# Performance work log

Measured on AMD Instinct MI355X. Metric: run time of the kernel, lower is better.

The kernel has to match this reference:

```python
import jax, jax.numpy as jnp
import numpy as np

VOCAB_SIZE = 32000
HIDDEN_DIM = 1024
NUM_BUF_ACTIONS = 128
BATCH = 64
SEQ_LEN = 512


def setup_inputs() -> dict:
    key = jax.random.key(0)
    ks = jax.random.split(key, 8)
    H = HIDDEN_DIM
    x = jax.random.randint(ks[0], (BATCH, SEQ_LEN), 0, VOCAB_SIZE, dtype=jnp.int32)
    true_actions = jax.random.randint(ks[1], (BATCH, SEQ_LEN), 0, NUM_BUF_ACTIONS, dtype=jnp.int32)
    true_states = jax.random.randint(ks[2], (BATCH, SEQ_LEN), 0, NUM_BUF_ACTIONS, dtype=jnp.int32)
    use_forcing = 0
    # Learned params: embedding table, LSTM input/recurrent kernels (gate order i,f,g,o), dense head
    embed = jax.random.normal(ks[3], (VOCAB_SIZE, H), dtype=jnp.float32) * 0.02
    Wi = jax.random.normal(ks[4], (H, 4 * H), dtype=jnp.float32) * (1.0 / np.sqrt(H))
    Wh = jax.random.normal(ks[5], (H, 4 * H), dtype=jnp.float32) * (1.0 / np.sqrt(H))
    bh = jnp.zeros((4 * H,), dtype=jnp.float32)
    Wo = jax.random.normal(ks[6], (H, NUM_BUF_ACTIONS), dtype=jnp.float32) * (1.0 / np.sqrt(H))
    bo = jnp.zeros((NUM_BUF_ACTIONS,), dtype=jnp.float32)
    return {"embed": embed, "Wi": Wi, "Wh": Wh, "bh": bh, "Wo": Wo, "bo": bo,
            "x": x, "true_actions": true_actions, "true_states": true_states,
            "use_forcing": use_forcing}


def _lstm_forward(embed, Wi, Wh, bh, Wo, bo, x):
    B, S = x.shape
    H = embed.shape[1]
    x_emb = embed[x]                                    # [B,S,H]
    # Precompute input-side gate projections for all timesteps (one big GEMM)
    gx = jnp.einsum('bsh,hg->sbg', x_emb, Wi)           # [S,B,4H]
    c0 = jnp.zeros((B, H), dtype=x_emb.dtype)
    h0 = jnp.zeros((B, H), dtype=x_emb.dtype)

    def step(carry, gx_t):
        c, h = carry
        gates = gx_t + h @ Wh + bh                      # [B,4H]
        i, f, g, o = jnp.split(gates, 4, axis=-1)
        i = jax.nn.sigmoid(i)
        f = jax.nn.sigmoid(f)
        g = jnp.tanh(g)
        o = jax.nn.sigmoid(o)
        c = f * c + i * g
        h = o * jnp.tanh(c)
        return (c, h), h

    _, hs = jax.lax.scan(step, (c0, h0), gx)            # hs: [S,B,H]
    hs = jnp.transpose(hs, (1, 0, 2))                   # [B,S,H]
    logits_buf = hs @ Wo + bo                           # [B,S,A]
    dummy = jnp.zeros((B, S, 1), dtype=logits_buf.dtype)
    return dummy, logits_buf, dummy


def reference(embed, Wi, Wh, bh, Wo, bo, x, true_actions, true_states, use_forcing):
    # true_actions/true_states/use_forcing are unused in the original forward
    return _lstm_forward(embed, Wi, Wh, bh, Wo, bo, x)
```

## Files before the change

### kernel.cpp

```cpp
#include <hip/hip_runtime.h>
#include <hip/hip_bf16.h>

typedef __attribute__((ext_vector_type(8))) short short8;
typedef __attribute__((ext_vector_type(4))) float float4v;
typedef __attribute__((ext_vector_type(4))) unsigned int uint4v;
typedef unsigned short ushort_t;
typedef unsigned int uint_t;

#define BB 64
#define SS 512
#define HH 1024
#define AA 128
#define NWG 256

#define XSW_BYTES   67108864ULL
#define WSW_BYTES   16777216ULL
#define HALL_BYTES  67239936ULL
#define XSW_OFF     0ULL
#define WSW_OFF     (XSW_OFF + XSW_BYTES)
#define HALL_OFF    (WSW_OFF + WSW_BYTES)
#define FLAGS_OFF   (HALL_OFF + HALL_BYTES)

__device__ __forceinline__ ushort_t f2bf(float f) {
    union { float f; uint_t u; } v; v.f = f;
    uint_t u = v.u;
    return (ushort_t)((u + 0x7fffu + ((u >> 16) & 1u)) >> 16);
}

__device__ __forceinline__ float fast_sigmoid(float x) {
    return __builtin_amdgcn_rcpf(1.0f + __expf(-x));
}
__device__ __forceinline__ float fast_tanh(float x) {
    return 1.0f - 2.0f * __builtin_amdgcn_rcpf(1.0f + __expf(2.0f * x));
}

__global__ void k_init(uint_t* __restrict__ flags, ushort_t* __restrict__ hall,
                       float* __restrict__ out) {
    int i = blockIdx.x * 256 + threadIdx.x;
    if (i < NWG) flags[i] = 0u;
    ((uint_t*)hall)[i] = 0u;
    out[i] = 0.0f;
    out[32768 + (size_t)BB * SS * AA + i] = 0.0f;
}

__global__ void k_prep_x(const float* __restrict__ embed, const int* __restrict__ x,
                         ushort_t* __restrict__ xsw) {
    int t = blockIdx.x * 256 + threadIdx.x;
    int lane = t & 63;
    int rg   = (t >> 6) & 3;
    int kk   = (t >> 8) & 31;
    int s    = t >> 13;
    int b  = rg * 16 + (lane & 15);
    int k0 = kk * 32 + (lane >> 4) * 8;
    int tok = x[b * SS + s];
    const float* src = embed + (size_t)tok * HH + k0;
    float4v v0 = *(const float4v*)src;
    float4v v1 = *(const float4v*)(src + 4);
    uint_t p0 = (uint_t)f2bf(v0[0]) | ((uint_t)f2bf(v0[1]) << 16);
    uint_t p1 = (uint_t)f2bf(v0[2]) | ((uint_t)f2bf(v0[3]) << 16);
    uint_t p2 = (uint_t)f2bf(v1[0]) | ((uint_t)f2bf(v1[1]) << 16);
    uint_t p3 = (uint_t)f2bf(v1[2]) | ((uint_t)f2bf(v1[3]) << 16);
    uint4v pk = {p0, p1, p2, p3};
    ((uint4v*)xsw)[t] = pk;
}

__global__ void k_prep_w(const float* __restrict__ Wi, const float* __restrict__ Wh,
                         ushort_t* __restrict__ wsw) {
    int t = blockIdx.x * 256 + threadIdx.x;
    int u = t & 1023;
    int q = (t >> 10) & 3;
    int k = t >> 12;
    float v = (k < 1024) ? Wi[(size_t)k * 4096 + q * 1024 + u]
                         : Wh[(size_t)(k - 1024) * 4096 + q * 1024 + u];
    int g = u >> 2, du = u & 3;
    int c = du * 4 + q;
    int kk = k >> 5, quad = (k >> 3) & 3, j = k & 7;
    int lane = quad * 16 + c;
    wsw[(((size_t)g * 64 + kk) * 64 + lane) * 8 + j] = f2bf(v);
}

__global__ void __launch_bounds__(256)
k_lstm(const ushort_t* __restrict__ xsw, const ushort_t* __restrict__ wsw,
       ushort_t* hall, const float* __restrict__ bh, uint_t* flags) {
    __shared__ ushort_t wlds[64 * 64 * 8];
    const int g    = blockIdx.x;
    const int tid  = threadIdx.x;
    const int lane = tid & 63;
    const int rg   = tid >> 6;

    {
        const uint4v* src = (const uint4v*)(wsw + (size_t)g * 64 * 64 * 8);
        uint4v* dst = (uint4v*)wlds;
        for (int i = tid; i < 4096; i += 256) dst[i] = src[i];
    }
    __syncthreads();

    const int c_idx = lane & 15;
    const int q  = c_idx & 3;
    const int du = c_idx >> 2;
    const int quad = lane >> 4;
    const int u = g * 4 + du;
    const float bhv = bh[q * 1024 + u];

    const int kk_h = u >> 5;
    const int quad_h = (u & 31) >> 3;
    const int j_h = u & 7;
    uint_t* hall32 = (uint_t*)hall;

    float cst0 = 0.f, cst1 = 0.f, cst2 = 0.f, cst3 = 0.f;
    const short8* xbase = (const short8*)xsw;
    const short8* hbase = (const short8*)hall;
    const short8* wl = (const short8*)wlds + lane;

    for (int s = 0; s < SS; ++s) {
        float4v ac0 = {bhv, bhv, bhv, bhv};
        float4v ac1 = {0.f, 0.f, 0.f, 0.f};
        float4v ac2 = {0.f, 0.f, 0.f, 0.f};
        float4v ac3 = {0.f, 0.f, 0.f, 0.f};

        const short8* xp = xbase + (((size_t)s * 32) * 4 + rg) * 64 + lane;
        #pragma unroll
        for (int kk = 0; kk < 32; kk += 4) {
            short8 a0 = xp[(kk + 0) * 256];
            short8 a1 = xp[(kk + 1) * 256];
            short8 a2 = xp[(kk + 2) * 256];
            short8 a3 = xp[(kk + 3) * 256];
            ac0 = __builtin_amdgcn_mfma_f32_16x16x32_bf16(a0, wl[(kk + 0) * 64], ac0, 0, 0, 0);
            ac1 = __builtin_amdgcn_mfma_f32_16x16x32_bf16(a1, wl[(kk + 1) * 64], ac1, 0, 0, 0);
            ac2 = __builtin_amdgcn_mfma_f32_16x16x32_bf16(a2, wl[(kk + 2) * 64], ac2, 0, 0, 0);
            ac3 = __builtin_amdgcn_mfma_f32_16x16x32_bf16(a3, wl[(kk + 3) * 64], ac3, 0, 0, 0);
        }

        {
            bool ok;
            do {
                uint_t f = __hip_atomic_load(&flags[tid], __ATOMIC_RELAXED,
                                             __HIP_MEMORY_SCOPE_AGENT);
                ok = (f >= (uint_t)s);
            } while (!__syncthreads_and(ok));
            asm volatile("" ::: "memory");
        }

        const short8* hp = hbase + (((size_t)s * 32) * 4 + rg) * 64 + lane;
        #pragma unroll
        for (int kk = 0; kk < 32; kk += 4) {
            short8 a0 = hp[(kk + 0) * 256];
            short8 a1 = hp[(kk + 1) * 256];
            short8 a2 = hp[(kk + 2) * 256];
            short8 a3 = hp[(kk + 3) * 256];
            ac0 = __builtin_amdgcn_mfma_f32_16x16x32_bf16(a0, wl[(32 + kk + 0) * 64], ac0, 0, 0, 0);
            ac1 = __builtin_amdgcn_mfma_f32_16x16x32_bf16(a1, wl[(32 + kk + 1) * 64], ac1, 0, 0, 0);
            ac2 = __builtin_amdgcn_mfma_f32_16x16x32_bf16(a2, wl[(32 + kk + 2) * 64], ac2, 0, 0, 0);
            ac3 = __builtin_amdgcn_mfma_f32_16x16x32_bf16(a3, wl[(32 + kk + 3) * 64], ac3, 0, 0, 0);
        }
        float4v acc = (ac0 + ac1) + (ac2 + ac3);

        float hv[4];
        #pragma unroll
        for (int r = 0; r < 4; ++r) {
            float own = acc[r];
            float a = (q == 2) ? fast_tanh(own) : fast_sigmoid(own);
            float x1 = __shfl_xor(a, 1);
            float x2 = __shfl_xor(a, 2);
            float x3 = __shfl_xor(a, 3);
            float gi, gf, gg, go;
            if      (q == 0) { gi = a;  gf = x1; gg = x2; go = x3; }
            else if (q == 1) { gi = x1; gf = a;  gg = x3; go = x2; }
            else if (q == 2) { gi = x2; gf = x3; gg = a;  go = x1; }
            else             { gi = x3; gf = x2; gg = x1; go = a;  }
            float cv = (r == 0 ? cst0 : r == 1 ? cst1 : r == 2 ? cst2 : cst3);
            cv = gf * cv + gi * gg;
            if (r == 0) cst0 = cv; else if (r == 1) cst1 = cv;
            else if (r == 2) cst2 = cv; else cst3 = cv;
            hv[r] = go * fast_tanh(cv);
        }

        float pv0 = __shfl_xor(hv[0], 4);
        float pv1 = __shfl_xor(hv[1], 4);
        float pv2 = __shfl_xor(hv[2], 4);
        float pv3 = __shfl_xor(hv[3], 4);
        if (q == 0 && (du & 1) == 0) {
            float pv[4] = {pv0, pv1, pv2, pv3};
            size_t base = (((size_t)(s + 1) * 32 + kk_h) * 4 + rg) * 64;
            #pragma unroll
            for (int r = 0; r < 4; ++r) {
                uint_t packed = (uint_t)f2bf(hv[r]) | ((uint_t)f2bf(pv[r]) << 16);
                int lane_h = quad_h * 16 + quad * 4 + r;
                size_t idx = ((base + (size_t)lane_h) * 8 + j_h) >> 1;
                __hip_atomic_store(&hall32[idx], packed, __ATOMIC_RELAXED,
                                   __HIP_MEMORY_SCOPE_AGENT);
            }
        }
        __syncthreads();
        if (tid == 0)
            __hip_atomic_store(&flags[g], (uint_t)(s + 1), __ATOMIC_RELAXED,
                               __HIP_MEMORY_SCOPE_AGENT);
    }
}

__global__ void __launch_bounds__(256)
k_head(const ushort_t* __restrict__ hall, const float* __restrict__ Wo,
       const float* __restrict__ bo, float* __restrict__ out) {
    __shared__ ushort_t wlds[32 * 2 * 64 * 8];
    const int wg = blockIdx.x;
    const int cg = wg & 3, sg = wg >> 2;
    const int tid = threadIdx.x, lane = tid & 63, rg = tid >> 6;
    const int col0 = cg * 32;

    for (int i = tid; i < 32768; i += 256) {
        int k = i >> 5;
        int col = i & 31;
        float v = Wo[(size_t)k * AA + col0 + col];
        int kk = k >> 5, quad = (k >> 3) & 3, j = k & 7;
        int nt = col >> 4, cl = col & 15;
        wlds[(((kk * 2 + nt) * 64) + quad * 16 + cl) * 8 + j] = f2bf(v);
    }
    __syncthreads();

    const int cl = lane & 15, quad = lane >> 4;
    const float bo0 = bo[col0 + cl];
    const float bo1 = bo[col0 + 16 + cl];
    const short8* wl = (const short8*)wlds + lane;

    for (int si = 0; si < 4; ++si) {
        int s = sg * 4 + si;
        float4v a0 = {bo0, bo0, bo0, bo0};
        float4v a1 = {bo1, bo1, bo1, bo1};
        const short8* hp = (const short8*)hall + (((size_t)(s + 1) * 32) * 4 + rg) * 64 + lane;
        #pragma unroll 8
        for (int kk = 0; kk < 32; ++kk) {
            short8 a = hp[kk * 256];
            a0 = __builtin_amdgcn_mfma_f32_16x16x32_bf16(a, wl[(kk * 2 + 0) * 64], a0, 0, 0, 0);
            a1 = __builtin_amdgcn_mfma_f32_16x16x32_bf16(a, wl[(kk * 2 + 1) * 64], a1, 0, 0, 0);
        }
        #pragma unroll
        for (int r = 0; r < 4; ++r) {
            int b = rg * 16 + quad * 4 + r;
            size_t o = 32768 + ((size_t)b * SS + s) * AA;
            out[o + col0 + cl]      = a0[r];
            out[o + col0 + 16 + cl] = a1[r];
        }
    }
}

extern "C" void kernel_launch(void* const* d_in, const int* in_sizes, int n_in,
                              void* d_out, int out_size, void* d_ws, size_t ws_size,
                              hipStream_t stream) {
    const float* embed = (const float*)d_in[0];
    const float* Wi    = (const float*)d_in[1];
    const float* Wh    = (const float*)d_in[2];
    const float* bh    = (const float*)d_in[3];
    const float* Wo    = (const float*)d_in[4];
    const float* bo    = (const float*)d_in[5];
    const int*   x     = (const int*)d_in[6];
    float* out = (float*)d_out;
    unsigned char* ws = (unsigned char*)d_ws;

    ushort_t* xsw  = (ushort_t*)(ws + XSW_OFF);
    ushort_t* wsw  = (ushort_t*)(ws + WSW_OFF);
    ushort_t* hall = (ushort_t*)(ws + HALL_OFF);
    uint_t*   flags = (uint_t*)(ws + FLAGS_OFF);

    k_init  <<<128,   256, 0, stream>>>(flags, hall, out);
    k_prep_x<<<16384, 256, 0, stream>>>(embed, x, xsw);
    k_prep_w<<<32768, 256, 0, stream>>>(Wi, Wh, wsw);
    k_lstm  <<<NWG,   256, 0, stream>>>(xsw, wsw, hall, bh, flags);
    k_head  <<<512,   256, 0, stream>>>(hall, Wo, bo, out);
}
```

Baseline: 2.804 ms.

## Hoist input-gate projection out of recurrent LSTM loop into a parallel GEMM kernel

The x·Wi projection moves out of the persistent recurrent kernel into a new fully parallel k_gx kernel that writes precomputed gate pre-activations, with bias folded in, as bf16 to workspace. The recurrent kernel now loads only the Wh half of the weights into LDS. Each step it just loads the precomputed gx slice and does the h·Wh MFMAs, which shortens the serial per-step work. The cost is an extra ~256MB bf16 round trip through memory, one more kernel launch, and an additional bf16 rounding of the input projection.

```diff
diff --git a/kernel.cpp b/kernel.cpp
--- a/kernel.cpp
+++ b/kernel.cpp
@@ -4,6 +4,7 @@
 typedef __attribute__((ext_vector_type(8))) short short8;
 typedef __attribute__((ext_vector_type(4))) float float4v;
 typedef __attribute__((ext_vector_type(4))) unsigned int uint4v;
+typedef __attribute__((ext_vector_type(2))) unsigned int uint2v;
 typedef unsigned short ushort_t;
 typedef unsigned int uint_t;
 
@@ -16,17 +17,27 @@
 #define XSW_BYTES   67108864ULL
 #define WSW_BYTES   16777216ULL
 #define HALL_BYTES  67239936ULL
+#define FLAG_BYTES  4096ULL
+#define GXW_BYTES   268435456ULL
 #define XSW_OFF     0ULL
 #define WSW_OFF     (XSW_OFF + XSW_BYTES)
 #define HALL_OFF    (WSW_OFF + WSW_BYTES)
 #define FLAGS_OFF   (HALL_OFF + HALL_BYTES)
+#define GXW_OFF     (FLAGS_OFF + FLAG_BYTES)
+
+#define GX_SSTRIDE  65536ULL
 
 __device__ __forceinline__ ushort_t f2bf(float f) {
     union { float f; uint_t u; } v; v.f = f;
     uint_t u = v.u;
     return (ushort_t)((u + 0x7fffu + ((u >> 16) & 1u)) >> 16);
 }
-
+__device__ __forceinline__ float bf_lo(uint_t w) {
+    union { uint_t u; float f; } v; v.u = w << 16; return v.f;
+}
+__device__ __forceinline__ float bf_hi(uint_t w) {
+    union { uint_t u; float f; } v; v.u = w & 0xffff0000u; return v.f;
+}
 __device__ __forceinline__ float fast_sigmoid(float x) {
     return __builtin_amdgcn_rcpf(1.0f + __expf(-x));
 }
@@ -34,11 +45,11 @@
     return 1.0f - 2.0f * __builtin_amdgcn_rcpf(1.0f + __expf(2.0f * x));
 }
 
-__global__ void k_init(uint_t* __restrict__ flags, ushort_t* __restrict__ hall,
+__global__ void k_init(uint_t* __restrict__ flags, uint_t* __restrict__ hall32,
                        float* __restrict__ out) {
     int i = blockIdx.x * 256 + threadIdx.x;
     if (i < NWG) flags[i] = 0u;
-    ((uint_t*)hall)[i] = 0u;
+    hall32[i] = 0u;
     out[i] = 0.0f;
     out[32768 + (size_t)BB * SS * AA + i] = 0.0f;
 }
@@ -80,44 +91,31 @@
 }
 
 __global__ void __launch_bounds__(256)
-k_lstm(const ushort_t* __restrict__ xsw, const ushort_t* __restrict__ wsw,
-       ushort_t* hall, const float* __restrict__ bh, uint_t* flags) {
-    __shared__ ushort_t wlds[64 * 64 * 8];
-    const int g    = blockIdx.x;
-    const int tid  = threadIdx.x;
-    const int lane = tid & 63;
-    const int rg   = tid >> 6;
+k_gx(const ushort_t* __restrict__ xsw, const ushort_t* __restrict__ wsw,
+     const float* __restrict__ bh, uint_t* __restrict__ gxw) {
+    __shared__ ushort_t wlds[32 * 64 * 8];
+    const int bx = blockIdx.x;
+    const int g = bx & 255;
+    const int sblk = bx >> 8;
+    const int tid = threadIdx.x, lane = tid & 63, rg = tid >> 6;
 
     {
         const uint4v* src = (const uint4v*)(wsw + (size_t)g * 64 * 64 * 8);
         uint4v* dst = (uint4v*)wlds;
-        for (int i = tid; i < 4096; i += 256) dst[i] = src[i];
+        for (int i = tid; i < 2048; i += 256) dst[i] = src[i];
     }
     __syncthreads();
 
     const int c_idx = lane & 15;
-    const int q  = c_idx & 3;
-    const int du = c_idx >> 2;
-    const int quad = lane >> 4;
-    const int u = g * 4 + du;
-    const float bhv = bh[q * 1024 + u];
-
-    const int kk_h = u >> 5;
-    const int quad_h = (u & 31) >> 3;
-    const int j_h = u & 7;
-    uint_t* hall32 = (uint_t*)hall;
-
-    float cst0 = 0.f, cst1 = 0.f, cst2 = 0.f, cst3 = 0.f;
+    const int q = c_idx & 3, du = c_idx >> 2;
+    const float bhv = bh[q * 1024 + (g * 4 + du)];
+    const short8* wl = (const short8*)wlds + lane;
     const short8* xbase = (const short8*)xsw;
-    const short8* hbase = (const short8*)hall;
-    const short8* wl = (const short8*)wlds + lane;
-
-    for (int s = 0; s < SS; ++s) {
-        float4v ac0 = {bhv, bhv, bhv, bhv};
-        float4v ac1 = {0.f, 0.f, 0.f, 0.f};
-        float4v ac2 = {0.f, 0.f, 0.f, 0.f};
-        float4v ac3 = {0.f, 0.f, 0.f, 0.f};
-
+
+    for (int si = 0; si < 8; ++si) {
+        int s = sblk * 8 + si;
+        float4v ac0 = {0.f,0.f,0.f,0.f}, ac1 = {0.f,0.f,0.f,0.f};
+        float4v ac2 = {0.f,0.f,0.f,0.f}, ac3 = {0.f,0.f,0.f,0.f};
         const short8* xp = xbase + (((size_t)s * 32) * 4 + rg) * 64 + lane;
         #pragma unroll
         for (int kk = 0; kk < 32; kk += 4) {
@@ -130,6 +128,49 @@
             ac2 = __builtin_amdgcn_mfma_f32_16x16x32_bf16(a2, wl[(kk + 2) * 64], ac2, 0, 0, 0);
             ac3 = __builtin_amdgcn_mfma_f32_16x16x32_bf16(a3, wl[(kk + 3) * 64], ac3, 0, 0, 0);
         }
+        float4v acc = (ac0 + ac1) + (ac2 + ac3);
+        uint_t w0 = (uint_t)f2bf(acc[0] + bhv) | ((uint_t)f2bf(acc[1] + bhv) << 16);
+        uint_t w1 = (uint_t)f2bf(acc[2] + bhv) | ((uint_t)f2bf(acc[3] + bhv) << 16);
+        uint2v pk = {w0, w1};
+        size_t o = (((size_t)s * 256 + g) * 4 + rg) * 64 + lane;
+        ((uint2v*)gxw)[o] = pk;
+    }
+}
+
+__global__ void __launch_bounds__(256, 1)
+k_lstm(const uint_t* __restrict__ gxw, const ushort_t* __restrict__ wsw,
+       ushort_t* hall, uint_t* flags) {
+    __shared__ ushort_t wlds[32 * 64 * 8];
+    const int g    = blockIdx.x;
+    const int tid  = threadIdx.x;
+    const int lane = tid & 63;
+    const int rg   = tid >> 6;
+
+    {
+        const uint4v* src = (const uint4v*)(wsw + (size_t)g * 64 * 64 * 8) + 2048;
+        uint4v* dst = (uint4v*)wlds;
+        for (int i = tid; i < 2048; i += 256) dst[i] = src[i];
+    }
+    __syncthreads();
+
+    const int c_idx = lane & 15;
+    const int q  = c_idx & 3;
+    const int du = c_idx >> 2;
+    const int quad = lane >> 4;
+    const int u = g * 4 + du;
+
+    const int kk_h = u >> 5;
+    const int quad_h = (u & 31) >> 3;
+    const int j_h = u & 7;
+    uint_t* hall32 = (uint_t*)hall;
+
+    float cst0 = 0.f, cst1 = 0.f, cst2 = 0.f, cst3 = 0.f;
+    const short8* hbase = (const short8*)hall;
+    const short8* wl = (const short8*)wlds + lane;
+    const uint2v* gxp = (const uint2v*)gxw + ((size_t)g * 4 + rg) * 64 + lane;
+
+    for (int s = 0; s < SS; ++s) {
+        uint2v gx = gxp[(size_t)s * GX_SSTRIDE];
 
         {
             bool ok;
@@ -141,6 +182,8 @@
             asm volatile("" ::: "memory");
         }
 
+        float4v ac0 = {0.f,0.f,0.f,0.f}, ac1 = {0.f,0.f,0.f,0.f};
+        float4v ac2 = {0.f,0.f,0.f,0.f}, ac3 = {0.f,0.f,0.f,0.f};
         const short8* hp = hbase + (((size_t)s * 32) * 4 + rg) * 64 + lane;
         #pragma unroll
         for (int kk = 0; kk < 32; kk += 4) {
@@ -148,12 +191,16 @@
             short8 a1 = hp[(kk + 1) * 256];
             short8 a2 = hp[(kk + 2) * 256];
             short8 a3 = hp[(kk + 3) * 256];
-            ac0 = __builtin_amdgcn_mfma_f32_16x16x32_bf16(a0, wl[(32 + kk + 0) * 64], ac0, 0, 0, 0);
-            ac1 = __builtin_amdgcn_mfma_f32_16x16x32_bf16(a1, wl[(32 + kk + 1) * 64], ac1, 0, 0, 0);
-            ac2 = __builtin_amdgcn_mfma_f32_16x16x32_bf16(a2, wl[(32 + kk + 2) * 64], ac2, 0, 0, 0);
-            ac3 = __builtin_amdgcn_mfma_f32_16x16x32_bf16(a3, wl[(32 + kk + 3) * 64], ac3, 0, 0, 0);
+            ac0 = __builtin_amdgcn_mfma_f32_16x16x32_bf16(a0, wl[(kk + 0) * 64], ac0, 0, 0, 0);
+            ac1 = __builtin_amdgcn_mfma_f32_16x16x32_bf16(a1, wl[(kk + 1) * 64], ac1, 0, 0, 0);
+            ac2 = __builtin_amdgcn_mfma_f32_16x16x32_bf16(a2, wl[(kk + 2) * 64], ac2, 0, 0, 0);
+            ac3 = __builtin_amdgcn_mfma_f32_16x16x32_bf16(a3, wl[(kk + 3) * 64], ac3, 0, 0, 0);
         }
         float4v acc = (ac0 + ac1) + (ac2 + ac3);
+        acc[0] += bf_lo(gx[0]);
+        acc[1] += bf_hi(gx[0]);
+        acc[2] += bf_lo(gx[1]);
+        acc[3] += bf_hi(gx[1]);
 
         float hv[4];
         #pragma unroll
@@ -260,10 +307,12 @@
     ushort_t* wsw  = (ushort_t*)(ws + WSW_OFF);
     ushort_t* hall = (ushort_t*)(ws + HALL_OFF);
     uint_t*   flags = (uint_t*)(ws + FLAGS_OFF);
-
-    k_init  <<<128,   256, 0, stream>>>(flags, hall, out);
+    uint_t*   gxw  = (uint_t*)(ws + GXW_OFF);
+
+    k_init  <<<128,   256, 0, stream>>>(flags, (uint_t*)hall, out);
     k_prep_x<<<16384, 256, 0, stream>>>(embed, x, xsw);
     k_prep_w<<<32768, 256, 0, stream>>>(Wi, Wh, wsw);
-    k_lstm  <<<NWG,   256, 0, stream>>>(xsw, wsw, hall, bh, flags);
+    k_gx    <<<16384, 256, 0, stream>>>(xsw, wsw, bh, gxw);
+    k_lstm  <<<NWG,   256, 0, stream>>>(gxw, wsw, hall, flags);
     k_head  <<<512,   256, 0, stream>>>(hall, Wo, bo, out);
 }
```

After: 4.858 ms. +73.2%, slower.
